# Performance work log

Measured on AMD Instinct MI355X. Metric: run time of the kernel, lower is better.

The kernel has to match this reference:

```python
import jax, jax.numpy as jnp
import numpy as np
from jax.scipy.stats import norm

N = 6144
D1, D2 = 3000, 1000
H = 128          # hardcoded hidden in VAEEncoder
LAT = 64
E = 16           # num_experts
K = 2            # top-k
NOISE_EPS = 0.01
BN_EPS = 1e-5


def setup_inputs() -> dict:
    key = jax.random.key(0)
    ks = jax.random.split(key, 24)
    xav = lambda k, i, o: jax.random.uniform(k, (i, o), jnp.float32,
                                             -np.sqrt(6.0 / (i + o)), np.sqrt(6.0 / (i + o)))
    u = jax.random.uniform(ks[0], (N, N), jnp.float32)
    adj = u / u.sum(axis=1, keepdims=True)  # row-normalized dense graph
    inp = {
        'x1': jax.random.normal(ks[1], (N, D1), jnp.float32),
        'x2': jax.random.normal(ks[2], (N, D2), jnp.float32),
        'adj': adj,
        # modality-1 VAE encoder
        'W1': xav(ks[3], D1, H), 'gamma1': jnp.ones((H,)), 'beta1': jnp.zeros((H,)),
        'Wmu1': xav(ks[4], H, LAT), 'bmu1': jnp.zeros((LAT,)),
        'Wlv1': xav(ks[5], H, LAT), 'blv1': jnp.zeros((LAT,)),
        # modality-2 VAE encoder
        'W2': xav(ks[6], D2, H), 'gamma2': jnp.ones((H,)), 'beta2': jnp.zeros((H,)),
        'Wmu2': xav(ks[7], H, LAT), 'bmu2': jnp.zeros((LAT,)),
        'Wlv2': xav(ks[8], H, LAT), 'blv2': jnp.zeros((LAT,)),
        # MoE gating (torch inits these to zero; small randn gives a non-degenerate baseline)
        'w_gate': 0.02 * jax.random.normal(ks[9], (LAT, E), jnp.float32),
        'w_noise': 0.02 * jax.random.normal(ks[10], (LAT, E), jnp.float32),
        # modality decoders
        'Wd1': xav(ks[11], LAT, LAT), 'Wfc1': xav(ks[12], LAT, D1), 'bfc1': jnp.zeros((D1,)),
        'Wd2': xav(ks[13], LAT, LAT), 'Wfc2': xav(ks[14], LAT, D2), 'bfc2': jnp.zeros((D2,)),
    }
    return inp


def _encode(x, adj, W, gamma, beta, Wmu, bmu, Wlv, blv):
    h = adj @ (x @ W)                                   # [N,H] GNN embed
    mu_b = h.mean(0)
    var_b = h.var(0)
    h = (h - mu_b) / jnp.sqrt(var_b + BN_EPS) * gamma + beta  # BatchNorm1d (train mode)
    return h @ Wmu + bmu, h @ Wlv + blv                 # mu, logvar [N,LAT]


def _cv_squared(v):
    return v.var(ddof=1) / (v.mean() ** 2 + 1e-10)


def _moe_gating(z, w_gate, w_noise, key):
    clean = z @ w_gate                                  # [N,E]
    std = jax.nn.softplus(z @ w_noise) + NOISE_EPS
    noisy = clean + jax.random.normal(key, clean.shape, clean.dtype) * std
    top_vals, top_idx = jax.lax.top_k(noisy, K + 1)     # [N,K+1]
    topk_gates = jax.nn.softmax(top_vals[:, :K], axis=1)
    rows = jnp.arange(z.shape[0])[:, None]
    gates = jnp.zeros_like(clean).at[rows, top_idx[:, :K]].set(topk_gates)
    # differentiable load estimate (prob each expert is in top-k)
    thr_in = top_vals[:, K][:, None]
    thr_out = top_vals[:, K - 1][:, None]
    is_in = noisy > thr_in
    prob = jnp.where(is_in, norm.cdf((clean - thr_in) / std), norm.cdf((clean - thr_out) / std))
    load = prob.sum(0)
    importance = gates.sum(0)
    loss = _cv_squared(importance) + _cv_squared(load)
    return gates, loss


def _decode(z, adj, Wd, Wfc, bfc):
    return (adj @ (z @ Wd)) @ Wfc + bfc                 # Decoder: mm, mm, Linear


def reference(x1, x2, adj,
              W1, gamma1, beta1, Wmu1, bmu1, Wlv1, blv1,
              W2, gamma2, beta2, Wmu2, bmu2, Wlv2, blv2,
              w_gate, w_noise,
              Wd1, Wfc1, bfc1, Wd2, Wfc2, bfc2):
    mu1, lv1 = _encode(x1, adj, W1, gamma1, beta1, Wmu1, bmu1, Wlv1, blv1)
    mu2, lv2 = _encode(x2, adj, W2, gamma2, beta2, Wmu2, bmu2, Wlv2, blv2)
    # Product of Experts over the 2 modalities
    mus = jnp.stack([mu1, mu2], 0)
    lvs = jnp.stack([lv1, lv2], 0)
    var = jnp.exp(lvs) + 1e-8
    T = 1.0 / (var + 1e-8)
    pd_mu = (mus * T).sum(0) / T.sum(0)
    pd_logvar = jnp.log(1.0 / T.sum(0) + 1e-8)
    z = pd_mu
    gates, moe_loss = _moe_gating(z, w_gate, w_noise, jax.random.key(42))
    recon1 = _decode(z, adj, Wd1, Wfc1, bfc1)
    recon2 = _decode(z, adj, Wd2, Wfc2, bfc2)
    return recon1, recon2, pd_mu, pd_logvar, gates, moe_loss
```

## Files before the change

### kernel.cpp

```cpp
#include <hip/hip_runtime.h>
#include <math.h>

#define NR    6144
#define DIM1  3000
#define DIM2  1000
#define HID   128
#define LATD  64
#define NEXP  16

typedef __bf16 bf16x8 __attribute__((ext_vector_type(8)));
typedef float  f32x4  __attribute__((ext_vector_type(4)));

__device__ __forceinline__ unsigned short f2bf_rne(float x) {
  unsigned u = __float_as_uint(x);
  u += 0x7FFFu + ((u >> 16) & 1u);
  return (unsigned short)(u >> 16);
}
__device__ __forceinline__ void split2(float v, unsigned short& h, unsigned short& l) {
  h = f2bf_rne(v);
  float hf = __uint_as_float((unsigned)h << 16);
  l = f2bf_rne(v - hf);
}
__device__ __forceinline__ unsigned cvt_pk_bf16(float a, float b) {
  unsigned r;
  asm("v_cvt_pk_bf16_f32 %0, %1, %2" : "=v"(r) : "v"(a), "v"(b));
  return r;
}

template<bool SPLIT3, bool ATOMIC>
__device__ __forceinline__ void gemm_body(
    unsigned short* __restrict__ bufA, unsigned short* __restrict__ bufB,
    const float* __restrict__ A,
    const unsigned short* __restrict__ BTh,
    const unsigned short* __restrict__ BTl,
    const float* __restrict__ bias,
    float* __restrict__ C,
    int M, int N, int K, int lda, int Kpad, int ldc,
    int bm, int bn, int k0, int kend)
{
  const int tid  = threadIdx.x;
  const int lane = tid & 63;
  const int wave = tid >> 6;
  const int wm = wave >> 1, wn = wave & 1;
  const int lrow = lane & 15, kg = lane >> 4;
  const int nsteps = (kend - k0 + 31) >> 5;

  f32x4 acc[4][4];
  #pragma unroll
  for (int f = 0; f < 4; ++f)
    #pragma unroll
    for (int g = 0; g < 4; ++g)
      #pragma unroll
      for (int j = 0; j < 4; ++j) acc[f][g][j] = 0.f;

  const int srow = tid >> 1;
  const int ks   = (tid & 1) * 16;
  const int s0   = (tid & 1) * 2;
  const float* aRow = A + (size_t)(bm + srow) * lda;
  const int gn = bn + srow;
  const bool bvalid = gn < N;
  const unsigned short* bRowH = BTh + (size_t)(bvalid ? gn : 0) * Kpad;
  const unsigned short* bRowL = SPLIT3 ? (BTl + (size_t)(bvalid ? gn : 0) * Kpad) : BTh;

  const int rx = srow & 7;
  const int wa0 = srow * 64 + (((s0 + 0) ^ rx) * 8);
  const int wa1 = srow * 64 + (((s0 + 1) ^ rx) * 8);
  const int wa2 = srow * 64 + (((s0 + 4) ^ rx) * 8);
  const int wa3 = srow * 64 + (((s0 + 5) ^ rx) * 8);

  float va[16];
  uint4 bh0 = make_uint4(0,0,0,0), bh1 = bh0, bl0 = bh0, bl1 = bh0;

  auto loadA = [&](int gk) {
    const int kb = gk + ks;
    if (kb + 16 <= kend) {
      const float4* ap = (const float4*)(aRow + kb);
      #pragma unroll
      for (int q = 0; q < 4; ++q) {
        float4 f4 = ap[q];
        va[4*q+0] = f4.x; va[4*q+1] = f4.y; va[4*q+2] = f4.z; va[4*q+3] = f4.w;
      }
    } else {
      #pragma unroll
      for (int i = 0; i < 16; ++i) va[i] = (kb + i < kend) ? aRow[kb + i] : 0.f;
    }
  };
  auto loadB = [&](int gk) {
    if (bvalid) {
      const uint4* bp = (const uint4*)(bRowH + gk + ks);
      bh0 = bp[0]; bh1 = bp[1];
      if (SPLIT3) {
        const uint4* bq = (const uint4*)(bRowL + gk + ks);
        bl0 = bq[0]; bl1 = bq[1];
      }
    }
  };

  loadA(k0);
  loadB(k0);

  for (int s = 0; s < nsteps; ++s) {
    unsigned hw[8], lw[8];
    #pragma unroll
    for (int i = 0; i < 8; ++i) {
      hw[i] = cvt_pk_bf16(va[2*i], va[2*i+1]);
      if (SPLIT3) {
        const float h0 = __uint_as_float(hw[i] << 16);
        const float h1 = __uint_as_float(hw[i] & 0xFFFF0000u);
        lw[i] = cvt_pk_bf16(va[2*i] - h0, va[2*i+1] - h1);
      } else {
        lw[i] = 0;
      }
    }

    __syncthreads();
    *(uint4*)&bufA[wa0] = make_uint4(hw[0], hw[1], hw[2], hw[3]);
    *(uint4*)&bufA[wa1] = make_uint4(hw[4], hw[5], hw[6], hw[7]);
    if (SPLIT3) {
      *(uint4*)&bufA[wa2] = make_uint4(lw[0], lw[1], lw[2], lw[3]);
      *(uint4*)&bufA[wa3] = make_uint4(lw[4], lw[5], lw[6], lw[7]);
      *(uint4*)&bufB[wa0] = bh0;
      *(uint4*)&bufB[wa1] = bh1;
      *(uint4*)&bufB[wa2] = bl0;
      *(uint4*)&bufB[wa3] = bl1;
    } else {
      *(uint4*)&bufA[wa2] = bh0;
      *(uint4*)&bufA[wa3] = bh1;
    }
    __syncthreads();

    if (s + 1 < nsteps) {
      loadA(k0 + (s + 1) * 32);
      loadB(k0 + (s + 1) * 32);
    }

    bf16x8 afh[4], bfh[4], afl[4], bfl[4];
    #pragma unroll
    for (int f = 0; f < 4; ++f) {
      const int r = wm * 64 + f * 16 + lrow;
      afh[f] = *(const bf16x8*)&bufA[r * 64 + ((kg ^ (r & 7)) * 8)];
      if (SPLIT3) afl[f] = *(const bf16x8*)&bufA[r * 64 + (((4 + kg) ^ (r & 7)) * 8)];
      const int n = wn * 64 + f * 16 + lrow;
      if (SPLIT3) {
        bfh[f] = *(const bf16x8*)&bufB[n * 64 + ((kg ^ (n & 7)) * 8)];
        bfl[f] = *(const bf16x8*)&bufB[n * 64 + (((4 + kg) ^ (n & 7)) * 8)];
      } else {
        bfh[f] = *(const bf16x8*)&bufA[n * 64 + (((4 + kg) ^ (n & 7)) * 8)];
      }
    }
    #pragma unroll
    for (int f = 0; f < 4; ++f)
      #pragma unroll
      for (int g = 0; g < 4; ++g) {
        acc[f][g] = __builtin_amdgcn_mfma_f32_16x16x32_bf16(afh[f], bfh[g], acc[f][g], 0, 0, 0);
        if constexpr (SPLIT3) {
          acc[f][g] = __builtin_amdgcn_mfma_f32_16x16x32_bf16(afl[f], bfh[g], acc[f][g], 0, 0, 0);
          acc[f][g] = __builtin_amdgcn_mfma_f32_16x16x32_bf16(afh[f], bfl[g], acc[f][g], 0, 0, 0);
        }
      }
  }

  #pragma unroll
  for (int f = 0; f < 4; ++f) {
    #pragma unroll
    for (int g = 0; g < 4; ++g) {
      const int row0 = bm + wm * 64 + f * 16 + (lane >> 4) * 4;
      const int col  = bn + wn * 64 + g * 16 + (lane & 15);
      if (col < N) {
        #pragma unroll
        for (int j = 0; j < 4; ++j) {
          const size_t idx = (size_t)(row0 + j) * ldc + col;
          if (ATOMIC) atomicAdd(&C[idx], acc[f][g][j]);
          else        C[idx] = acc[f][g][j] + (bias ? bias[col] : 0.f);
        }
      }
    }
  }
}

template<bool SPLIT3, bool ATOMIC>
__global__ __launch_bounds__(256, 2) void gemm_mfma(
    const float* __restrict__ A,
    const unsigned short* __restrict__ BTh,
    const unsigned short* __restrict__ BTl,
    const float* __restrict__ bias,
    float* __restrict__ C,
    int M, int N, int K, int lda, int Kpad, int ldc, int kchunk)
{
  __shared__ alignas(16) unsigned short bufA[128 * 64];
  __shared__ alignas(16) unsigned short bufB[SPLIT3 ? 128 * 64 : 8];
  const int k0 = blockIdx.z * kchunk;
  gemm_body<SPLIT3, ATOMIC>(bufA, bufB, A, BTh, BTl, bias, C,
                            M, N, K, lda, Kpad, ldc,
                            blockIdx.x * 128, blockIdx.y * 128,
                            k0, min(k0 + kchunk, K));
}

__global__ __launch_bounds__(256, 2) void gemm_enc(
    const float* __restrict__ x1,
    const unsigned short* __restrict__ W1h, const unsigned short* __restrict__ W1l,
    const float* __restrict__ x2,
    const unsigned short* __restrict__ W2h, const unsigned short* __restrict__ W2l,
    float* __restrict__ XW)
{
  __shared__ alignas(16) unsigned short bufA[128 * 64];
  __shared__ alignas(16) unsigned short bufB[128 * 64];
  if (blockIdx.y == 0) {
    const int k0 = blockIdx.z * 192;
    if (k0 >= DIM1) return;
    gemm_body<true, true>(bufA, bufB, x1, W1h, W1l, nullptr, XW,
                          NR, HID, DIM1, DIM1, 3008, 256,
                          blockIdx.x * 128, 0, k0, min(k0 + 192, DIM1));
  } else {
    const int k0 = blockIdx.z * 64;
    if (k0 >= DIM2) return;
    gemm_body<true, true>(bufA, bufB, x2, W2h, W2l, nullptr, XW + HID,
                          NR, HID, DIM2, DIM2, 1024, 256,
                          blockIdx.x * 128, 0, k0, min(k0 + 64, DIM2));
  }
}

__global__ __launch_bounds__(256) void transpose_split(
    const float* __restrict__ in, unsigned short* __restrict__ out_hi,
    unsigned short* __restrict__ out_lo, int K, int N, int Kpad)
{
  __shared__ float tile[32][33];
  const int k0 = blockIdx.x * 32, n0 = blockIdx.y * 32;
  const int tx = threadIdx.x & 31, ty = threadIdx.x >> 5;
  #pragma unroll
  for (int r = 0; r < 4; ++r) {
    const int k = k0 + ty + r * 8;
    tile[ty + r * 8][tx] = (k < K && n0 + tx < N) ? in[(size_t)k * N + n0 + tx] : 0.f;
  }
  __syncthreads();
  #pragma unroll
  for (int r = 0; r < 4; ++r) {
    const int nn = ty + r * 8;
    const int n = n0 + nn, k = k0 + tx;
    if (n < N && k < Kpad) {
      unsigned short h, l;
      split2(tile[tx][nn], h, l);
      out_hi[(size_t)n * Kpad + k] = h;
      if (out_lo) out_lo[(size_t)n * Kpad + k] = l;
    }
  }
}

#define BM 64
#define BN 64
#define BK 16

__global__ __launch_bounds__(256) void gemm_f32(
    const float* __restrict__ A, const float* __restrict__ B,
    const float* __restrict__ bias, float* __restrict__ C,
    int M, int N, int K, int lda, int ldb, int ldc)
{
  __shared__ float At[BK][BM + 4];
  __shared__ float Bt[BK][BN + 4];
  const int tid = threadIdx.x;
  const int tx = tid & 15;
  const int ty = tid >> 4;
  const int bm = blockIdx.x * BM;
  const int bn = blockIdx.y * BN;

  float acc[4][4] = {};

  const int ar = tid >> 2;
  const int ak = (tid & 3) * 4;
  const int bk = tid >> 4;
  const int bc = (tid & 15) * 4;

  for (int k0 = 0; k0 < K; k0 += BK) {
    {
      float4 v = make_float4(0.f, 0.f, 0.f, 0.f);
      const int gr = bm + ar;
      const int gk = k0 + ak;
      if (gr < M && gk < K) {
        const float* p = &A[(size_t)gr * lda];
        if (gk + 3 < K) v = *reinterpret_cast<const float4*>(&p[gk]);
        else {
          v.x = p[gk];
          if (gk + 1 < K) v.y = p[gk + 1];
          if (gk + 2 < K) v.z = p[gk + 2];
        }
      }
      At[ak + 0][ar] = v.x; At[ak + 1][ar] = v.y;
      At[ak + 2][ar] = v.z; At[ak + 3][ar] = v.w;
    }
    {
      float4 v = make_float4(0.f, 0.f, 0.f, 0.f);
      const int gk = k0 + bk;
      const int gc = bn + bc;
      if (gk < K) {
        const float* p = &B[(size_t)gk * ldb];
        if (gc + 3 < N) v = *reinterpret_cast<const float4*>(&p[gc]);
        else {
          if (gc     < N) v.x = p[gc];
          if (gc + 1 < N) v.y = p[gc + 1];
          if (gc + 2 < N) v.z = p[gc + 2];
        }
      }
      *reinterpret_cast<float4*>(&Bt[bk][bc]) = v;
    }
    __syncthreads();
    #pragma unroll
    for (int kk = 0; kk < BK; ++kk) {
      float4 a4 = *reinterpret_cast<const float4*>(&At[kk][ty * 4]);
      float4 b4 = *reinterpret_cast<const float4*>(&Bt[kk][tx * 4]);
      float av[4] = {a4.x, a4.y, a4.z, a4.w};
      float bv[4] = {b4.x, b4.y, b4.z, b4.w};
      #pragma unroll
      for (int i = 0; i < 4; ++i)
        #pragma unroll
        for (int j = 0; j < 4; ++j)
          acc[i][j] = fmaf(av[i], bv[j], acc[i][j]);
    }
    __syncthreads();
  }

  #pragma unroll
  for (int i = 0; i < 4; ++i) {
    const int row = bm + ty * 4 + i;
    if (row >= M) continue;
    #pragma unroll
    for (int j = 0; j < 4; ++j) {
      const int col = bn + tx * 4 + j;
      if (col < N) {
        float v = acc[i][j];
        if (bias) v += bias[col];
        C[(size_t)row * ldc + col] = v;
      }
    }
  }
}

__global__ __launch_bounds__(256) void bnstats_kernel(
    const float* __restrict__ H2, float* __restrict__ ssum, float* __restrict__ ssq)
{
  const int c = threadIdx.x;
  const int r0 = blockIdx.x * 12;
  float s = 0.f, q = 0.f;
  #pragma unroll
  for (int i = 0; i < 12; ++i) {
    float v = H2[(size_t)(r0 + i) * 256 + c];
    s += v;
    q = fmaf(v, v, q);
  }
  atomicAdd(&ssum[c], s);
  atomicAdd(&ssq[c], q);
}

__global__ __launch_bounds__(256) void mulv_kernel(
    const float* __restrict__ H2, const float* __restrict__ ssum, const float* __restrict__ ssq,
    const float* __restrict__ g1, const float* __restrict__ b1,
    const float* __restrict__ Wmu1, const float* __restrict__ bmu1,
    const float* __restrict__ Wlv1, const float* __restrict__ blv1,
    const float* __restrict__ g2, const float* __restrict__ b2,
    const float* __restrict__ Wmu2, const float* __restrict__ bmu2,
    const float* __restrict__ Wlv2, const float* __restrict__ blv2,
    float* __restrict__ pd_mu_out, float* __restrict__ pd_lv_out, float* __restrict__ z_out)
{
  __shared__ float hn[4][256];
  const int tid = threadIdx.x;
  const int r0 = blockIdx.x * 4;

  for (int idx = tid; idx < 1024; idx += 256) {
    const int rr = idx >> 8;
    const int c  = idx & 255;
    const float mean = ssum[c] * (1.0f / 6144.0f);
    const float var  = ssq[c] * (1.0f / 6144.0f) - mean * mean;
    const float rstd = 1.0f / sqrtf(var + 1e-5f);
    const float gamma = (c < HID) ? g1[c] : g2[c - HID];
    const float beta  = (c < HID) ? b1[c] : b2[c - HID];
    const float v = H2[(size_t)(r0 + rr) * 256 + c];
    hn[rr][c] = (v - mean) * rstd * gamma + beta;
  }
  __syncthreads();

  const int rr = tid >> 6;
  const int j  = tid & 63;
  float mu1 = bmu1[j], lv1 = blv1[j], mu2 = bmu2[j], lv2 = blv2[j];
  #pragma unroll 4
  for (int k = 0; k < HID; ++k) {
    const float h1 = hn[rr][k];
    const float h2 = hn[rr][HID + k];
    mu1 = fmaf(h1, Wmu1[k * LATD + j], mu1);
    lv1 = fmaf(h1, Wlv1[k * LATD + j], lv1);
    mu2 = fmaf(h2, Wmu2[k * LATD + j], mu2);
    lv2 = fmaf(h2, Wlv2[k * LATD + j], lv2);
  }
  const float var1 = expf(lv1) + 1e-8f;
  const float var2 = expf(lv2) + 1e-8f;
  const float T1 = 1.0f / (var1 + 1e-8f);
  const float T2 = 1.0f / (var2 + 1e-8f);
  const float denom = T1 + T2;
  const float pmu = (mu1 * T1 + mu2 * T2) / denom;
  const float plv = logf(1.0f / denom + 1e-8f);
  const size_t o = (size_t)(r0 + rr) * LATD + j;
  pd_mu_out[o] = pmu;
  pd_lv_out[o] = plv;
  z_out[o]     = pmu;
}

__device__ __forceinline__ unsigned rotl32(unsigned x, int r) {
  return (x << r) | (x >> (32 - r));
}

__device__ float threefry_normal(unsigned i) {
  const unsigned ks0 = 0u;
  const unsigned ks1 = 42u;
  const unsigned ks2 = 0x1BD11BDAu ^ 0u ^ 42u;
  unsigned x0 = 0u + ks0;
  unsigned x1 = i + ks1;

  #define TF_ROUND(r) { x0 += x1; x1 = rotl32(x1, r); x1 ^= x0; }
  TF_ROUND(13) TF_ROUND(15) TF_ROUND(26) TF_ROUND(6)
  x0 += ks1; x1 += ks2 + 1u;
  TF_ROUND(17) TF_ROUND(29) TF_ROUND(16) TF_ROUND(24)
  x0 += ks2; x1 += ks0 + 2u;
  TF_ROUND(13) TF_ROUND(15) TF_ROUND(26) TF_ROUND(6)
  x0 += ks0; x1 += ks1 + 3u;
  TF_ROUND(17) TF_ROUND(29) TF_ROUND(16) TF_ROUND(24)
  x0 += ks1; x1 += ks2 + 4u;
  TF_ROUND(13) TF_ROUND(15) TF_ROUND(26) TF_ROUND(6)
  x0 += ks2; x1 += ks0 + 5u;
  #undef TF_ROUND

  const unsigned bits = x0 ^ x1;

  const unsigned fb = (bits >> 9) | 0x3F800000u;
  const float u01 = __uint_as_float(fb) - 1.0f;
  const float minval = -0.99999994f;
  float u = fmaf(u01, 2.0f, minval);
  u = fmaxf(minval, u);

  float w = -log1pf(-u * u);
  float p;
  if (w < 5.0f) {
    w = w - 2.5f;
    p = 2.81022636e-08f;
    p = fmaf(p, w, 3.43273939e-07f);
    p = fmaf(p, w, -3.5233877e-06f);
    p = fmaf(p, w, -4.39150654e-06f);
    p = fmaf(p, w, 0.00021858087f);
    p = fmaf(p, w, -0.00125372503f);
    p = fmaf(p, w, -0.00417768164f);
    p = fmaf(p, w, 0.246640727f);
    p = fmaf(p, w, 1.50140941f);
  } else {
    w = sqrtf(w) - 3.0f;
    p = -0.000200214257f;
    p = fmaf(p, w, 0.000100950558f);
    p = fmaf(p, w, 0.00134934322f);
    p = fmaf(p, w, -0.00367342844f);
    p = fmaf(p, w, 0.00573950773f);
    p = fmaf(p, w, -0.0076224613f);
    p = fmaf(p, w, 0.00943887047f);
    p = fmaf(p, w, 1.00167406f);
    p = fmaf(p, w, 2.83297682f);
  }
  return 1.4142135f * (p * u);
}

__global__ __launch_bounds__(64) void gating_kernel(
    const float* __restrict__ z, const float* __restrict__ w_gate,
    const float* __restrict__ w_noise, float* __restrict__ gates_out,
    float* __restrict__ importance, float* __restrict__ loadv)
{
  __shared__ float zt[64][65];
  __shared__ float wg[64][16];
  __shared__ float wn[64][16];
  __shared__ float imp_s[16];
  __shared__ float load_s[16];

  const int tid = threadIdx.x;
  const int r0 = blockIdx.x * 64;

  for (int idx = tid; idx < 1024; idx += 64) {
    wg[idx >> 4][idx & 15] = w_gate[idx];
    wn[idx >> 4][idx & 15] = w_noise[idx];
  }
  for (int idx = tid; idx < 4096; idx += 64) {
    const int rr = idx >> 6, c = idx & 63;
    zt[rr][c] = z[(size_t)(r0 + rr) * 64 + c];
  }
  if (tid < 16) { imp_s[tid] = 0.f; load_s[tid] = 0.f; }
  __syncthreads();

  const int r = r0 + tid;
  float clean[16], noisy[16], stdv[16];
  #pragma unroll
  for (int e = 0; e < NEXP; ++e) {
    float c = 0.f, n = 0.f;
    #pragma unroll 8
    for (int k = 0; k < 64; ++k) {
      const float zv = zt[tid][k];
      c = fmaf(zv, wg[k][e], c);
      n = fmaf(zv, wn[k][e], n);
    }
    clean[e] = c;
    const float sp = fmaxf(n, 0.f) + log1pf(expf(-fabsf(n)));
    stdv[e] = sp + 0.01f;
    const float eps = threefry_normal((unsigned)r * 16u + (unsigned)e);
    noisy[e] = fmaf(eps, stdv[e], c);
  }

  float v0 = -1e30f, v1 = -1e30f, v2 = -1e30f;
  int i0 = 0, i1 = 0;
  #pragma unroll
  for (int e = 0; e < NEXP; ++e) {
    const float v = noisy[e];
    if (v > v0)      { v2 = v1; v1 = v0; i1 = i0; v0 = v; i0 = e; }
    else if (v > v1) { v2 = v1; v1 = v; i1 = e; }
    else if (v > v2) { v2 = v; }
  }

  const float e1 = expf(v1 - v0);
  const float inv = 1.0f / (1.0f + e1);
  const float g0 = inv;
  const float g1v = e1 * inv;

  float lacc[16];
  #pragma unroll
  for (int e = 0; e < NEXP; ++e) {
    const float gv = (e == i0) ? g0 : ((e == i1) ? g1v : 0.f);
    gates_out[(size_t)r * NEXP + e] = gv;
    const float thr = (noisy[e] > v2) ? v2 : v1;
    const float x = (clean[e] - thr) / stdv[e];
    lacc[e] = 0.5f * erfcf(-0.70710678f * x);
  }
  atomicAdd(&imp_s[i0], g0);
  atomicAdd(&imp_s[i1], g1v);
  #pragma unroll
  for (int e = 0; e < NEXP; ++e) atomicAdd(&load_s[e], lacc[e]);
  __syncthreads();
  if (tid < 16) {
    atomicAdd(&importance[tid], imp_s[tid]);
    atomicAdd(&loadv[tid], load_s[tid]);
  }
}

__global__ void loss_kernel(const float* __restrict__ imp, const float* __restrict__ ld,
                            float* __restrict__ out)
{
  if (threadIdx.x == 0 && blockIdx.x == 0) {
    float mi = 0.f, ml = 0.f;
    for (int e = 0; e < NEXP; ++e) { mi += imp[e]; ml += ld[e]; }
    mi *= (1.0f / 16.0f);
    ml *= (1.0f / 16.0f);
    float vi = 0.f, vl = 0.f;
    for (int e = 0; e < NEXP; ++e) {
      const float di = imp[e] - mi;
      const float dl = ld[e] - ml;
      vi = fmaf(di, di, vi);
      vl = fmaf(dl, dl, vl);
    }
    vi *= (1.0f / 15.0f);
    vl *= (1.0f / 15.0f);
    out[0] = vi / (mi * mi + 1e-10f) + vl / (ml * ml + 1e-10f);
  }
}

extern "C" void kernel_launch(void* const* d_in, const int* in_sizes, int n_in,
                              void* d_out, int out_size, void* d_ws, size_t ws_size,
                              hipStream_t stream)
{
  const float* x1     = (const float*)d_in[0];
  const float* x2     = (const float*)d_in[1];
  const float* adj    = (const float*)d_in[2];
  const float* W1     = (const float*)d_in[3];
  const float* gamma1 = (const float*)d_in[4];
  const float* beta1  = (const float*)d_in[5];
  const float* Wmu1   = (const float*)d_in[6];
  const float* bmu1   = (const float*)d_in[7];
  const float* Wlv1   = (const float*)d_in[8];
  const float* blv1   = (const float*)d_in[9];
  const float* W2     = (const float*)d_in[10];
  const float* gamma2 = (const float*)d_in[11];
  const float* beta2  = (const float*)d_in[12];
  const float* Wmu2   = (const float*)d_in[13];
  const float* bmu2   = (const float*)d_in[14];
  const float* Wlv2   = (const float*)d_in[15];
  const float* blv2   = (const float*)d_in[16];
  const float* w_gate = (const float*)d_in[17];
  const float* w_noise= (const float*)d_in[18];
  const float* Wd1    = (const float*)d_in[19];
  const float* Wfc1   = (const float*)d_in[20];
  const float* bfc1   = (const float*)d_in[21];
  const float* Wd2    = (const float*)d_in[22];
  const float* Wfc2   = (const float*)d_in[23];
  const float* bfc2   = (const float*)d_in[24];

  float* out = (float*)d_out;
  float* recon1 = out;
  float* recon2 = out + (size_t)NR * DIM1;
  float* pd_mu  = recon2 + (size_t)NR * DIM2;
  float* pd_lv  = pd_mu + (size_t)NR * LATD;
  float* gates  = pd_lv + (size_t)NR * LATD;
  float* loss   = gates + (size_t)NR * NEXP;

  char* wsb = (char*)d_ws;
  const size_t o_XW   = 0;
  const size_t o_H2   = o_XW   + 6291456;
  const size_t o_z    = o_H2   + 6291456;
  const size_t o_ZD   = o_z    + 1572864;
  const size_t o_AZ   = o_ZD   + 3145728;
  const size_t o_XWTh = o_AZ   + 3145728;
  const size_t o_XWTl = o_XWTh + 3145728;
  const size_t o_W1Th = o_XWTl + 3145728;
  const size_t o_W1Tl = o_W1Th + 770048;
  const size_t o_W2Th = o_W1Tl + 770048;
  const size_t o_W2Tl = o_W2Th + 262144;
  const size_t o_ZDTh = o_W2Tl + 262144;
  const size_t o_F1Th = o_ZDTh + 1572864;
  const size_t o_F2Th = o_F1Th + 384000;
  const size_t o_stat = o_F2Th + 128000;
  const size_t need   = o_stat + 2176;

  const dim3 blk(256);

  if (ws_size >= need) {
    float* XW   = (float*)(wsb + o_XW);
    float* H2   = (float*)(wsb + o_H2);
    float* zbuf = (float*)(wsb + o_z);
    float* ZD   = (float*)(wsb + o_ZD);
    float* AZ   = (float*)(wsb + o_AZ);
    unsigned short* XWTh = (unsigned short*)(wsb + o_XWTh);
    unsigned short* XWTl = (unsigned short*)(wsb + o_XWTl);
    unsigned short* W1Th = (unsigned short*)(wsb + o_W1Th);
    unsigned short* W1Tl = (unsigned short*)(wsb + o_W1Tl);
    unsigned short* W2Th = (unsigned short*)(wsb + o_W2Th);
    unsigned short* W2Tl = (unsigned short*)(wsb + o_W2Tl);
    unsigned short* ZDTh = (unsigned short*)(wsb + o_ZDTh);
    unsigned short* F1Th = (unsigned short*)(wsb + o_F1Th);
    unsigned short* F2Th = (unsigned short*)(wsb + o_F2Th);
    float* ssum = (float*)(wsb + o_stat);
    float* ssq  = ssum + 256;
    float* imp  = ssq + 256;
    float* ldv  = imp + 16;

    hipMemsetAsync(XW, 0, 6291456 * 2, stream);
    hipMemsetAsync(AZ, 0, 3145728, stream);
    hipMemsetAsync(ssum, 0, 2176, stream);

    transpose_split<<<dim3(94, 4), blk, 0, stream>>>(W1, W1Th, W1Tl, DIM1, HID, 3008);
    transpose_split<<<dim3(32, 4), blk, 0, stream>>>(W2, W2Th, W2Tl, DIM2, HID, 1024);
    transpose_split<<<dim3(2, 94), blk, 0, stream>>>(Wfc1, F1Th, nullptr, LATD, DIM1, 64);
    transpose_split<<<dim3(2, 32), blk, 0, stream>>>(Wfc2, F2Th, nullptr, LATD, DIM2, 64);

    gemm_enc<<<dim3(48, 2, 16), blk, 0, stream>>>(x1, W1Th, W1Tl, x2, W2Th, W2Tl, XW);

    transpose_split<<<dim3(192, 8), blk, 0, stream>>>(XW, XWTh, XWTl, NR, 256, NR);

    gemm_mfma<true, true><<<dim3(48, 2, 16), blk, 0, stream>>>(
        adj, XWTh, XWTl, nullptr, H2, NR, 256, NR, NR, NR, 256, 384);

    bnstats_kernel<<<512, blk, 0, stream>>>(H2, ssum, ssq);
    mulv_kernel<<<NR / 4, blk, 0, stream>>>(H2, ssum, ssq,
        gamma1, beta1, Wmu1, bmu1, Wlv1, blv1,
        gamma2, beta2, Wmu2, bmu2, Wlv2, blv2,
        pd_mu, pd_lv, zbuf);

    gating_kernel<<<NR / 64, 64, 0, stream>>>(zbuf, w_gate, w_noise, gates, imp, ldv);
    loss_kernel<<<1, 64, 0, stream>>>(imp, ldv, loss);

    gemm_f32<<<dim3(96, 1), blk, 0, stream>>>(zbuf, Wd1, nullptr, ZD,        NR, LATD, LATD, LATD, LATD, 128);
    gemm_f32<<<dim3(96, 1), blk, 0, stream>>>(zbuf, Wd2, nullptr, ZD + LATD, NR, LATD, LATD, LATD, LATD, 128);
    transpose_split<<<dim3(192, 4), blk, 0, stream>>>(ZD, ZDTh, nullptr, NR, 128, NR);
    gemm_mfma<false, true><<<dim3(48, 1, 16), blk, 0, stream>>>(
        adj, ZDTh, nullptr, nullptr, AZ, NR, 128, NR, NR, NR, 128, 384);
    gemm_mfma<false, false><<<dim3(48, 24, 1), blk, 0, stream>>>(
        AZ, F1Th, nullptr, bfc1, recon1, NR, DIM1, LATD, 128, 64, DIM1, 64);
    gemm_mfma<false, false><<<dim3(48, 8, 1), blk, 0, stream>>>(
        AZ + LATD, F2Th, nullptr, bfc2, recon2, NR, DIM2, LATD, 128, 64, DIM2, 64);
    return;
  }

  float* ws   = (float*)d_ws;
  float* XW   = ws;
  float* H2   = ws + 1572864;
  float* zbuf = ws + 3145728;
  float* ZD   = ws + 3538944;
  float* AZ   = ws + 4325376;
  float* ssum = ws + 5111808;
  float* ssq  = ws + 5112064;
  float* imp  = ws + 5112320;
  float* ldv  = ws + 5112336;

  hipMemsetAsync(ssum, 0, 544 * sizeof(float), stream);

  gemm_f32<<<dim3(NR / BM, 2), blk, 0, stream>>>(x1, W1, nullptr, XW,        NR, HID, DIM1, DIM1, HID, 256);
  gemm_f32<<<dim3(NR / BM, 2), blk, 0, stream>>>(x2, W2, nullptr, XW + HID,  NR, HID, DIM2, DIM2, HID, 256);
  gemm_f32<<<dim3(NR / BM, 4), blk, 0, stream>>>(adj, XW, nullptr, H2, NR, 256, NR, NR, 256, 256);
  bnstats_kernel<<<512, blk, 0, stream>>>(H2, ssum, ssq);
  mulv_kernel<<<NR / 4, blk, 0, stream>>>(H2, ssum, ssq,
                                          gamma1, beta1, Wmu1, bmu1, Wlv1, blv1,
                                          gamma2, beta2, Wmu2, bmu2, Wlv2, blv2,
                                          pd_mu, pd_lv, zbuf);
  gating_kernel<<<NR / 64, 64, 0, stream>>>(zbuf, w_gate, w_noise, gates, imp, ldv);
  loss_kernel<<<1, 64, 0, stream>>>(imp, ldv, loss);
  gemm_f32<<<dim3(NR / BM, 1), blk, 0, stream>>>(zbuf, Wd1, nullptr, ZD,        NR, LATD, LATD, LATD, LATD, 128);
  gemm_f32<<<dim3(NR / BM, 1), blk, 0, stream>>>(zbuf, Wd2, nullptr, ZD + LATD, NR, LATD, LATD, LATD, LATD, 128);
  gemm_f32<<<dim3(NR / BM, 2), blk, 0, stream>>>(adj, ZD, nullptr, AZ, NR, 128, NR, NR, 128, 128);
  gemm_f32<<<dim3(NR / BM, (DIM1 + BN - 1) / BN), blk, 0, stream>>>(AZ,        Wfc1, bfc1, recon1, NR, DIM1, LATD, 128, DIM1, DIM1);
  gemm_f32<<<dim3(NR / BM, (DIM2 + BN - 1) / BN), blk, 0, stream>>>(AZ + LATD, Wfc2, bfc2, recon2, NR, DIM2, LATD, 128, DIM2, DIM2);
}
```

Baseline: 463.7 us.

## Pre-pack split-bf16 B tiles and stream them into LDS with global_load_lds

The split-precision GEMMs (encoder x@W and adj@XW) now take B operands pre-packed into swizzled 128x32 hi/lo tile images. These are copied straight into double-buffered LDS through global_load_lds, so B no longer goes through registers and ds_write. The split path gets its own kernel with a launch bound of 3 blocks per SM, and the K-chunks are doubled with half the z-splits, which cuts atomic traffic. The aim is to lower VGPR and LDS-write pressure and overlap B fetches with compute, at the cost of more LDS per block and a packing pass.

```diff
diff --git a/kernel.cpp b/kernel.cpp
--- a/kernel.cpp
+++ b/kernel.cpp
@@ -27,15 +27,12 @@
   return r;
 }
 
-template<bool SPLIT3, bool ATOMIC>
-__device__ __forceinline__ void gemm_body(
-    unsigned short* __restrict__ bufA, unsigned short* __restrict__ bufB,
-    const float* __restrict__ A,
-    const unsigned short* __restrict__ BTh,
-    const unsigned short* __restrict__ BTl,
-    const float* __restrict__ bias,
-    float* __restrict__ C,
-    int M, int N, int K, int lda, int Kpad, int ldc,
+template<bool ATOMIC>
+__device__ __forceinline__ void gemm_body3(
+    unsigned short* __restrict__ bufA,
+    unsigned short* __restrict__ bufB0, unsigned short* __restrict__ bufB1,
+    const float* __restrict__ A, const unsigned short* __restrict__ Bblk,
+    float* __restrict__ C, int N, int lda, int ldc,
     int bm, int bn, int k0, int kend)
 {
   const int tid  = threadIdx.x;
@@ -44,6 +41,203 @@
   const int wm = wave >> 1, wn = wave & 1;
   const int lrow = lane & 15, kg = lane >> 4;
   const int nsteps = (kend - k0 + 31) >> 5;
+  if (nsteps <= 0) return;
+
+  f32x4 acc[4][4];
+  #pragma unroll
+  for (int f = 0; f < 4; ++f)
+    #pragma unroll
+    for (int g = 0; g < 4; ++g)
+      #pragma unroll
+      for (int j = 0; j < 4; ++j) acc[f][g][j] = 0.f;
+
+  const int srow = tid >> 1;
+  const int ks   = (tid & 1) * 16;
+  const int s0   = (tid & 1) * 2;
+  const float* aRow = A + (size_t)(bm + srow) * lda;
+  const int rx = srow & 7;
+  const int wa0 = srow * 64 + (((s0 + 0) ^ rx) * 8);
+  const int wa1 = srow * 64 + (((s0 + 1) ^ rx) * 8);
+  const int wa2 = srow * 64 + (((s0 + 4) ^ rx) * 8);
+  const int wa3 = srow * 64 + (((s0 + 5) ^ rx) * 8);
+
+  float va[16];
+
+  #define LOAD_A(gk) {                                                  \
+    const int kb = (gk) + ks;                                           \
+    if (kb + 16 <= kend) {                                              \
+      const float4* ap = (const float4*)(aRow + kb);                    \
+      float4 f0 = ap[0], f1 = ap[1], f2 = ap[2], f3 = ap[3];            \
+      va[0]=f0.x; va[1]=f0.y; va[2]=f0.z; va[3]=f0.w;                   \
+      va[4]=f1.x; va[5]=f1.y; va[6]=f1.z; va[7]=f1.w;                   \
+      va[8]=f2.x; va[9]=f2.y; va[10]=f2.z; va[11]=f2.w;                 \
+      va[12]=f3.x; va[13]=f3.y; va[14]=f3.z; va[15]=f3.w;               \
+    } else {                                                            \
+      _Pragma("unroll")                                                 \
+      for (int i = 0; i < 16; ++i) va[i] = (kb + i < kend) ? aRow[kb + i] : 0.f; \
+    }                                                                   \
+  }
+
+  #define STAGE_B(gk, dst) {                                            \
+    const unsigned short* _src = Bblk + ((size_t)((gk) >> 5)) * 8192 + wave * 2048 + lane * 8; \
+    unsigned short* _d = (dst) + wave * 2048;                           \
+    __builtin_amdgcn_global_load_lds((const __attribute__((address_space(1))) unsigned int*)(_src),        (__attribute__((address_space(3))) unsigned int*)(_d),        16, 0, 0); \
+    __builtin_amdgcn_global_load_lds((const __attribute__((address_space(1))) unsigned int*)(_src + 512),  (__attribute__((address_space(3))) unsigned int*)(_d + 512),  16, 0, 0); \
+    __builtin_amdgcn_global_load_lds((const __attribute__((address_space(1))) unsigned int*)(_src + 1024), (__attribute__((address_space(3))) unsigned int*)(_d + 1024), 16, 0, 0); \
+    __builtin_amdgcn_global_load_lds((const __attribute__((address_space(1))) unsigned int*)(_src + 1536), (__attribute__((address_space(3))) unsigned int*)(_d + 1536), 16, 0, 0); \
+  }
+
+  LOAD_A(k0);
+  STAGE_B(k0, bufB0);
+
+  for (int s = 0; s < nsteps; ++s) {
+    unsigned short* bCur = (s & 1) ? bufB1 : bufB0;
+    unsigned short* bNxt = (s & 1) ? bufB0 : bufB1;
+
+    unsigned hw[8], lw[8];
+    #pragma unroll
+    for (int i = 0; i < 8; ++i) {
+      hw[i] = cvt_pk_bf16(va[2*i], va[2*i+1]);
+      const float h0 = __uint_as_float(hw[i] << 16);
+      const float h1 = __uint_as_float(hw[i] & 0xFFFF0000u);
+      lw[i] = cvt_pk_bf16(va[2*i] - h0, va[2*i+1] - h1);
+    }
+
+    __syncthreads();
+    *(uint4*)&bufA[wa0] = make_uint4(hw[0], hw[1], hw[2], hw[3]);
+    *(uint4*)&bufA[wa1] = make_uint4(hw[4], hw[5], hw[6], hw[7]);
+    *(uint4*)&bufA[wa2] = make_uint4(lw[0], lw[1], lw[2], lw[3]);
+    *(uint4*)&bufA[wa3] = make_uint4(lw[4], lw[5], lw[6], lw[7]);
+    __syncthreads();
+
+    if (s + 1 < nsteps) {
+      LOAD_A(k0 + (s + 1) * 32);
+      STAGE_B(k0 + (s + 1) * 32, bNxt);
+    }
+
+    bf16x8 afh[4], bfh[4], afl[4], bfl[4];
+    #pragma unroll
+    for (int f = 0; f < 4; ++f) {
+      const int r = wm * 64 + f * 16 + lrow;
+      afh[f] = *(const bf16x8*)&bufA[r * 64 + ((kg ^ (r & 7)) * 8)];
+      afl[f] = *(const bf16x8*)&bufA[r * 64 + (((4 + kg) ^ (r & 7)) * 8)];
+      const int n = wn * 64 + f * 16 + lrow;
+      bfh[f] = *(const bf16x8*)&bCur[n * 64 + ((kg ^ (n & 7)) * 8)];
+      bfl[f] = *(const bf16x8*)&bCur[n * 64 + (((4 + kg) ^ (n & 7)) * 8)];
+    }
+    #pragma unroll
+    for (int f = 0; f < 4; ++f)
+      #pragma unroll
+      for (int g = 0; g < 4; ++g) {
+        acc[f][g] = __builtin_amdgcn_mfma_f32_16x16x32_bf16(afh[f], bfh[g], acc[f][g], 0, 0, 0);
+        acc[f][g] = __builtin_amdgcn_mfma_f32_16x16x32_bf16(afl[f], bfh[g], acc[f][g], 0, 0, 0);
+        acc[f][g] = __builtin_amdgcn_mfma_f32_16x16x32_bf16(afh[f], bfl[g], acc[f][g], 0, 0, 0);
+      }
+  }
+  #undef LOAD_A
+  #undef STAGE_B
+
+  #pragma unroll
+  for (int f = 0; f < 4; ++f) {
+    #pragma unroll
+    for (int g = 0; g < 4; ++g) {
+      const int row0 = bm + wm * 64 + f * 16 + (lane >> 4) * 4;
+      const int col  = bn + wn * 64 + g * 16 + (lane & 15);
+      if (col < N) {
+        #pragma unroll
+        for (int j = 0; j < 4; ++j) {
+          const size_t idx = (size_t)(row0 + j) * ldc + col;
+          if (ATOMIC) atomicAdd(&C[idx], acc[f][g][j]);
+          else        C[idx] = acc[f][g][j];
+        }
+      }
+    }
+  }
+}
+
+template<bool ATOMIC>
+__global__ __launch_bounds__(256, 3) void gemm_mfma3(
+    const float* __restrict__ A, const unsigned short* __restrict__ Bblk,
+    int kblocks_per_tile, float* __restrict__ C,
+    int N, int lda, int ldc, int K, int kchunk)
+{
+  __shared__ alignas(16) unsigned short bufA[8192];
+  __shared__ alignas(16) unsigned short bufB0[8192];
+  __shared__ alignas(16) unsigned short bufB1[8192];
+  const unsigned short* Bt = Bblk + (size_t)blockIdx.y * kblocks_per_tile * 8192;
+  const int k0 = blockIdx.z * kchunk;
+  gemm_body3<ATOMIC>(bufA, bufB0, bufB1, A, Bt, C, N, lda, ldc,
+                     blockIdx.x * 128, blockIdx.y * 128, k0, min(k0 + kchunk, K));
+}
+
+__global__ __launch_bounds__(256, 3) void gemm_enc3(
+    const float* __restrict__ x1, const unsigned short* __restrict__ W1blk,
+    const float* __restrict__ x2, const unsigned short* __restrict__ W2blk,
+    float* __restrict__ XW)
+{
+  __shared__ alignas(16) unsigned short bufA[8192];
+  __shared__ alignas(16) unsigned short bufB0[8192];
+  __shared__ alignas(16) unsigned short bufB1[8192];
+  if (blockIdx.y == 0) {
+    const int k0 = blockIdx.z * 384;
+    gemm_body3<true>(bufA, bufB0, bufB1, x1, W1blk, XW, HID, DIM1, 256,
+                     blockIdx.x * 128, 0, k0, min(k0 + 384, DIM1));
+  } else {
+    const int k0 = blockIdx.z * 128;
+    gemm_body3<true>(bufA, bufB0, bufB1, x2, W2blk, XW + HID, HID, DIM2, 256,
+                     blockIdx.x * 128, 0, k0, min(k0 + 128, DIM2));
+  }
+}
+
+__global__ __launch_bounds__(256) void pack_b_blocks(
+    const float* __restrict__ in, int K, int ldin, int col0,
+    unsigned short* __restrict__ out)
+{
+  __shared__ unsigned short img[8192];
+  const int tid = threadIdx.x;
+  const int ks  = blockIdx.x;
+  const int k0  = ks * 32;
+  const int c   = tid & 127;
+  const int h   = tid >> 7;
+  const int colg = col0 + blockIdx.y * 128 + c;
+  #pragma unroll
+  for (int i = 0; i < 16; ++i) {
+    const int kl = h + 2 * i;
+    const int k  = k0 + kl;
+    const float v = (k < K) ? in[(size_t)k * ldin + colg] : 0.f;
+    unsigned short hi, lo;
+    split2(v, hi, lo);
+    const int base = c * 64 + (kl & 7);
+    img[base + (((kl >> 3) ^ (c & 7)) * 8)]       = hi;
+    img[base + ((((kl >> 3) + 4) ^ (c & 7)) * 8)] = lo;
+  }
+  __syncthreads();
+  const size_t ob = ((size_t)blockIdx.y * gridDim.x + ks) * 8192;
+  const uint4* s4 = (const uint4*)img;
+  uint4* o4 = (uint4*)(out + ob);
+  #pragma unroll
+  for (int i = 0; i < 4; ++i) o4[tid + i * 256] = s4[tid + i * 256];
+}
+
+template<bool ATOMIC>
+__global__ __launch_bounds__(256, 3) void gemm_mfma1(
+    const float* __restrict__ A,
+    const unsigned short* __restrict__ BT,
+    const float* __restrict__ bias,
+    float* __restrict__ C,
+    int M, int N, int K, int lda, int Kpad, int ldc, int kchunk)
+{
+  __shared__ alignas(16) unsigned short bufA[128 * 64];
+  const int tid  = threadIdx.x;
+  const int lane = tid & 63;
+  const int wave = tid >> 6;
+  const int wm = wave >> 1, wn = wave & 1;
+  const int lrow = lane & 15, kg = lane >> 4;
+  const int bm = blockIdx.x * 128;
+  const int bn = blockIdx.y * 128;
+  const int k0 = blockIdx.z * kchunk;
+  const int kend = min(k0 + kchunk, K);
+  const int nsteps = (kend - k0 + 31) >> 5;
 
   f32x4 acc[4][4];
   #pragma unroll
@@ -59,9 +253,7 @@
   const float* aRow = A + (size_t)(bm + srow) * lda;
   const int gn = bn + srow;
   const bool bvalid = gn < N;
-  const unsigned short* bRowH = BTh + (size_t)(bvalid ? gn : 0) * Kpad;
-  const unsigned short* bRowL = SPLIT3 ? (BTl + (size_t)(bvalid ? gn : 0) * Kpad) : BTh;
-
+  const unsigned short* bRowH = BT + (size_t)(bvalid ? gn : 0) * Kpad;
   const int rx = srow & 7;
   const int wa0 = srow * 64 + (((s0 + 0) ^ rx) * 8);
   const int wa1 = srow * 64 + (((s0 + 1) ^ rx) * 8);
@@ -69,96 +261,66 @@
   const int wa3 = srow * 64 + (((s0 + 5) ^ rx) * 8);
 
   float va[16];
-  uint4 bh0 = make_uint4(0,0,0,0), bh1 = bh0, bl0 = bh0, bl1 = bh0;
-
-  auto loadA = [&](int gk) {
-    const int kb = gk + ks;
-    if (kb + 16 <= kend) {
-      const float4* ap = (const float4*)(aRow + kb);
-      #pragma unroll
-      for (int q = 0; q < 4; ++q) {
-        float4 f4 = ap[q];
-        va[4*q+0] = f4.x; va[4*q+1] = f4.y; va[4*q+2] = f4.z; va[4*q+3] = f4.w;
-      }
-    } else {
-      #pragma unroll
-      for (int i = 0; i < 16; ++i) va[i] = (kb + i < kend) ? aRow[kb + i] : 0.f;
-    }
-  };
-  auto loadB = [&](int gk) {
-    if (bvalid) {
-      const uint4* bp = (const uint4*)(bRowH + gk + ks);
-      bh0 = bp[0]; bh1 = bp[1];
-      if (SPLIT3) {
-        const uint4* bq = (const uint4*)(bRowL + gk + ks);
-        bl0 = bq[0]; bl1 = bq[1];
-      }
-    }
-  };
-
-  loadA(k0);
-  loadB(k0);
+  uint4 bh0 = make_uint4(0,0,0,0), bh1 = bh0;
+
+  #define LOAD_A1(gk) {                                                 \
+    const int kb = (gk) + ks;                                           \
+    if (kb + 16 <= kend) {                                              \
+      const float4* ap = (const float4*)(aRow + kb);                    \
+      float4 f0 = ap[0], f1 = ap[1], f2 = ap[2], f3 = ap[3];            \
+      va[0]=f0.x; va[1]=f0.y; va[2]=f0.z; va[3]=f0.w;                   \
+      va[4]=f1.x; va[5]=f1.y; va[6]=f1.z; va[7]=f1.w;                   \
+      va[8]=f2.x; va[9]=f2.y; va[10]=f2.z; va[11]=f2.w;                 \
+      va[12]=f3.x; va[13]=f3.y; va[14]=f3.z; va[15]=f3.w;               \
+    } else {                                                            \
+      _Pragma("unroll")                                                 \
+      for (int i = 0; i < 16; ++i) va[i] = (kb + i < kend) ? aRow[kb + i] : 0.f; \
+    }                                                                   \
+  }
+  #define LOAD_B1(gk) {                                                 \
+    if (bvalid) {                                                       \
+      const uint4* bp = (const uint4*)(bRowH + (gk) + ks);              \
+      bh0 = bp[0]; bh1 = bp[1];                                         \
+    }                                                                   \
+  }
+
+  LOAD_A1(k0);
+  LOAD_B1(k0);
 
   for (int s = 0; s < nsteps; ++s) {
-    unsigned hw[8], lw[8];
-    #pragma unroll
-    for (int i = 0; i < 8; ++i) {
-      hw[i] = cvt_pk_bf16(va[2*i], va[2*i+1]);
-      if (SPLIT3) {
-        const float h0 = __uint_as_float(hw[i] << 16);
-        const float h1 = __uint_as_float(hw[i] & 0xFFFF0000u);
-        lw[i] = cvt_pk_bf16(va[2*i] - h0, va[2*i+1] - h1);
-      } else {
-        lw[i] = 0;
-      }
-    }
+    unsigned hw[8];
+    #pragma unroll
+    for (int i = 0; i < 8; ++i) hw[i] = cvt_pk_bf16(va[2*i], va[2*i+1]);
+    uint4 wb0 = bh0, wb1 = bh1;
 
     __syncthreads();
     *(uint4*)&bufA[wa0] = make_uint4(hw[0], hw[1], hw[2], hw[3]);
     *(uint4*)&bufA[wa1] = make_uint4(hw[4], hw[5], hw[6], hw[7]);
-    if (SPLIT3) {
-      *(uint4*)&bufA[wa2] = make_uint4(lw[0], lw[1], lw[2], lw[3]);
-      *(uint4*)&bufA[wa3] = make_uint4(lw[4], lw[5], lw[6], lw[7]);
-      *(uint4*)&bufB[wa0] = bh0;
-      *(uint4*)&bufB[wa1] = bh1;
-      *(uint4*)&bufB[wa2] = bl0;
-      *(uint4*)&bufB[wa3] = bl1;
-    } else {
-      *(uint4*)&bufA[wa2] = bh0;
-      *(uint4*)&bufA[wa3] = bh1;
-    }
+    *(uint4*)&bufA[wa2] = wb0;
+    *(uint4*)&bufA[wa3] = wb1;
     __syncthreads();
 
     if (s + 1 < nsteps) {
-      loadA(k0 + (s + 1) * 32);
-      loadB(k0 + (s + 1) * 32);
-    }
-
-    bf16x8 afh[4], bfh[4], afl[4], bfl[4];
+      LOAD_A1(k0 + (s + 1) * 32);
+      LOAD_B1(k0 + (s + 1) * 32);
+    }
+
+    bf16x8 afh[4], bfh[4];
     #pragma unroll
     for (int f = 0; f < 4; ++f) {
       const int r = wm * 64 + f * 16 + lrow;
       afh[f] = *(const bf16x8*)&bufA[r * 64 + ((kg ^ (r & 7)) * 8)];
-      if (SPLIT3) afl[f] = *(const bf16x8*)&bufA[r * 64 + (((4 + kg) ^ (r & 7)) * 8)];
       const int n = wn * 64 + f * 16 + lrow;
-      if (SPLIT3) {
-        bfh[f] = *(const bf16x8*)&bufB[n * 64 + ((kg ^ (n & 7)) * 8)];
-        bfl[f] = *(const bf16x8*)&bufB[n * 64 + (((4 + kg) ^ (n & 7)) * 8)];
-      } else {
-        bfh[f] = *(const bf16x8*)&bufA[n * 64 + (((4 + kg) ^ (n & 7)) * 8)];
-      }
+      bfh[f] = *(const bf16x8*)&bufA[n * 64 + (((4 + kg) ^ (n & 7)) * 8)];
     }
     #pragma unroll
     for (int f = 0; f < 4; ++f)
       #pragma unroll
-      for (int g = 0; g < 4; ++g) {
+      for (int g = 0; g < 4; ++g)
         acc[f][g] = __builtin_amdgcn_mfma_f32_16x16x32_bf16(afh[f], bfh[g], acc[f][g], 0, 0, 0);
-        if constexpr (SPLIT3) {
-          acc[f][g] = __builtin_amdgcn_mfma_f32_16x16x32_bf16(afl[f], bfh[g], acc[f][g], 0, 0, 0);
-          acc[f][g] = __builtin_amdgcn_mfma_f32_16x16x32_bf16(afh[f], bfl[g], acc[f][g], 0, 0, 0);
-        }
-      }
-  }
+  }
+  #undef LOAD_A1
+  #undef LOAD_B1
 
   #pragma unroll
   for (int f = 0; f < 4; ++f) {
@@ -175,48 +337,6 @@
         }
       }
     }
-  }
-}
-
-template<bool SPLIT3, bool ATOMIC>
-__global__ __launch_bounds__(256, 2) void gemm_mfma(
-    const float* __restrict__ A,
-    const unsigned short* __restrict__ BTh,
-    const unsigned short* __restrict__ BTl,
-    const float* __restrict__ bias,
-    float* __restrict__ C,
-    int M, int N, int K, int lda, int Kpad, int ldc, int kchunk)
-{
-  __shared__ alignas(16) unsigned short bufA[128 * 64];
-  __shared__ alignas(16) unsigned short bufB[SPLIT3 ? 128 * 64 : 8];
-  const int k0 = blockIdx.z * kchunk;
-  gemm_body<SPLIT3, ATOMIC>(bufA, bufB, A, BTh, BTl, bias, C,
-                            M, N, K, lda, Kpad, ldc,
-                            blockIdx.x * 128, blockIdx.y * 128,
-                            k0, min(k0 + kchunk, K));
-}
-
-__global__ __launch_bounds__(256, 2) void gemm_enc(
-    const float* __restrict__ x1,
-    const unsigned short* __restrict__ W1h, const unsigned short* __restrict__ W1l,
-    const float* __restrict__ x2,
-    const unsigned short* __restrict__ W2h, const unsigned short* __restrict__ W2l,
-    float* __restrict__ XW)
-{
-  __shared__ alignas(16) unsigned short bufA[128 * 64];
-  __shared__ alignas(16) unsigned short bufB[128 * 64];
-  if (blockIdx.y == 0) {
-    const int k0 = blockIdx.z * 192;
-    if (k0 >= DIM1) return;
-    gemm_body<true, true>(bufA, bufB, x1, W1h, W1l, nullptr, XW,
-                          NR, HID, DIM1, DIM1, 3008, 256,
-                          blockIdx.x * 128, 0, k0, min(k0 + 192, DIM1));
-  } else {
-    const int k0 = blockIdx.z * 64;
-    if (k0 >= DIM2) return;
-    gemm_body<true, true>(bufA, bufB, x2, W2h, W2l, nullptr, XW + HID,
-                          NR, HID, DIM2, DIM2, 1024, 256,
-                          blockIdx.x * 128, 0, k0, min(k0 + 64, DIM2));
   }
 }
 
@@ -605,13 +725,10 @@
   const size_t o_z    = o_H2   + 6291456;
   const size_t o_ZD   = o_z    + 1572864;
   const size_t o_AZ   = o_ZD   + 3145728;
-  const size_t o_XWTh = o_AZ   + 3145728;
-  const size_t o_XWTl = o_XWTh + 3145728;
-  const size_t o_W1Th = o_XWTl + 3145728;
-  const size_t o_W1Tl = o_W1Th + 770048;
-  const size_t o_W2Th = o_W1Tl + 770048;
-  const size_t o_W2Tl = o_W2Th + 262144;
-  const size_t o_ZDTh = o_W2Tl + 262144;
+  const size_t o_XWB  = o_AZ   + 3145728;
+  const size_t o_W1B  = o_XWB  + 6291456;
+  const size_t o_W2B  = o_W1B  + 1540096;
+  const size_t o_ZDTh = o_W2B  + 524288;
   const size_t o_F1Th = o_ZDTh + 1572864;
   const size_t o_F2Th = o_F1Th + 384000;
   const size_t o_stat = o_F2Th + 128000;
@@ -625,12 +742,9 @@
     float* zbuf = (float*)(wsb + o_z);
     float* ZD   = (float*)(wsb + o_ZD);
     float* AZ   = (float*)(wsb + o_AZ);
-    unsigned short* XWTh = (unsigned short*)(wsb + o_XWTh);
-    unsigned short* XWTl = (unsigned short*)(wsb + o_XWTl);
-    unsigned short* W1Th = (unsigned short*)(wsb + o_W1Th);
-    unsigned short* W1Tl = (unsigned short*)(wsb + o_W1Tl);
-    unsigned short* W2Th = (unsigned short*)(wsb + o_W2Th);
-    unsigned short* W2Tl = (unsigned short*)(wsb + o_W2Tl);
+    unsigned short* XWB  = (unsigned short*)(wsb + o_XWB);
+    unsigned short* W1B  = (unsigned short*)(wsb + o_W1B);
+    unsigned short* W2B  = (unsigned short*)(wsb + o_W2B);
     unsigned short* ZDTh = (unsigned short*)(wsb + o_ZDTh);
     unsigned short* F1Th = (unsigned short*)(wsb + o_F1Th);
     unsigned short* F2Th = (unsigned short*)(wsb + o_F2Th);
@@ -643,17 +757,17 @@
     hipMemsetAsync(AZ, 0, 3145728, stream);
     hipMemsetAsync(ssum, 0, 2176, stream);
 
-    transpose_split<<<dim3(94, 4), blk, 0, stream>>>(W1, W1Th, W1Tl, DIM1, HID, 3008);
-    transpose_split<<<dim3(32, 4), blk, 0, stream>>>(W2, W2Th, W2Tl, DIM2, HID, 1024);
+    pack_b_blocks<<<dim3(94, 1), blk, 0, stream>>>(W1, DIM1, HID, 0, W1B);
+    pack_b_blocks<<<dim3(32, 1), blk, 0, stream>>>(W2, DIM2, HID, 0, W2B);
     transpose_split<<<dim3(2, 94), blk, 0, stream>>>(Wfc1, F1Th, nullptr, LATD, DIM1, 64);
     transpose_split<<<dim3(2, 32), blk, 0, stream>>>(Wfc2, F2Th, nullptr, LATD, DIM2, 64);
 
-    gemm_enc<<<dim3(48, 2, 16), blk, 0, stream>>>(x1, W1Th, W1Tl, x2, W2Th, W2Tl, XW);
-
-    transpose_split<<<dim3(192, 8), blk, 0, stream>>>(XW, XWTh, XWTl, NR, 256, NR);
-
-    gemm_mfma<true, true><<<dim3(48, 2, 16), blk, 0, stream>>>(
-        adj, XWTh, XWTl, nullptr, H2, NR, 256, NR, NR, NR, 256, 384);
+    gemm_enc3<<<dim3(48, 2, 8), blk, 0, stream>>>(x1, W1B, x2, W2B, XW);
+
+    pack_b_blocks<<<dim3(192, 2), blk, 0, stream>>>(XW, NR, 256, 0, XWB);
+
+    gemm_mfma3<true><<<dim3(48, 2, 8), blk, 0, stream>>>(
+        adj, XWB, 192, H2, 256, NR, 256, NR, 768);
 
     bnstats_kernel<<<512, blk, 0, stream>>>(H2, ssum, ssq);
     mulv_kernel<<<NR / 4, blk, 0, stream>>>(H2, ssum, ssq,
@@ -667,12 +781,12 @@
     gemm_f32<<<dim3(96, 1), blk, 0, stream>>>(zbuf, Wd1, nullptr, ZD,        NR, LATD, LATD, LATD, LATD, 128);
     gemm_f32<<<dim3(96, 1), blk, 0, stream>>>(zbuf, Wd2, nullptr, ZD + LATD, NR, LATD, LATD, LATD, LATD, 128);
     transpose_split<<<dim3(192, 4), blk, 0, stream>>>(ZD, ZDTh, nullptr, NR, 128, NR);
-    gemm_mfma<false, true><<<dim3(48, 1, 16), blk, 0, stream>>>(
-        adj, ZDTh, nullptr, nullptr, AZ, NR, 128, NR, NR, NR, 128, 384);
-    gemm_mfma<false, false><<<dim3(48, 24, 1), blk, 0, stream>>>(
-        AZ, F1Th, nullptr, bfc1, recon1, NR, DIM1, LATD, 128, 64, DIM1, 64);
-    gemm_mfma<false, false><<<dim3(48, 8, 1), blk, 0, stream>>>(
-        AZ + LATD, F2Th, nullptr, bfc2, recon2, NR, DIM2, LATD, 128, 64, DIM2, 64);
+    gemm_mfma1<true><<<dim3(48, 1, 16), blk, 0, stream>>>(
+        adj, ZDTh, nullptr, AZ, NR, 128, NR, NR, NR, 128, 384);
+    gemm_mfma1<false><<<dim3(48, 24, 1), blk, 0, stream>>>(
+        AZ, F1Th, bfc1, recon1, NR, DIM1, LATD, 128, 64, DIM1, 64);
+    gemm_mfma1<false><<<dim3(48, 8, 1), blk, 0, stream>>>(
+        AZ + LATD, F2Th, bfc2, recon2, NR, DIM2, LATD, 128, 64, DIM2, 64);
     return;
   }
 
```

Result: faster. 415.2 us (-10.5%).
